# Performance work log

Measured on AMD Instinct MI355X. Metric: run time of the kernel, lower is better.

Reference implementation:

```python
import jax, jax.numpy as jnp
import numpy as np

LN_EPS = 1e-3  # keras LayerNormalization default


def setup_inputs() -> dict:
    key = jax.random.key(0)
    k1, k2, k3 = jax.random.split(key, 3)
    B, T, D, H = 64, 512, 256, 512
    inputs = jax.random.normal(k1, (B, T, D), dtype=jnp.float32)
    h0 = jnp.zeros((B, H), dtype=jnp.float32)
    Wx = jax.random.normal(k2, (D, H), dtype=jnp.float32) / np.sqrt(D)
    Wh = jax.random.normal(k3, (H, H), dtype=jnp.float32) / np.sqrt(H)
    b = jnp.zeros((H,), dtype=jnp.float32)
    gamma = jnp.ones((H,), dtype=jnp.float32)
    beta = jnp.zeros((H,), dtype=jnp.float32)
    return {"inputs": inputs, "h0": h0, "Wx": Wx, "Wh": Wh, "b": b,
            "gamma": gamma, "beta": beta}


def _layer_norm(x, gamma, beta):
    mu = jnp.mean(x, axis=-1, keepdims=True)
    var = jnp.mean(jnp.square(x - mu), axis=-1, keepdims=True)
    return (x - mu) * jax.lax.rsqrt(var + LN_EPS) * gamma + beta


def reference(inputs, h0, Wx, Wh, b, gamma, beta):
    # Precompute input projection for all timesteps: [B, T, H]
    xproj = jnp.einsum('btd,dh->bth', inputs, Wx) + b

    def step(h, xp_t):
        z = xp_t + h @ Wh                      # SimpleRNNCell, activation=None
        h_new = jnp.tanh(_layer_norm(z, gamma, beta))
        return h_new, h_new

    _, outs = jax.lax.scan(step, h0, jnp.swapaxes(xproj, 0, 1))
    return jnp.swapaxes(outs, 0, 1)            # [B, T, H]
```

## Files before the change

kernel.cpp:

```cpp
#include <hip/hip_runtime.h>
#include <cstdint>
#include <cstddef>

#define T_STEPS 512
#define D_DIM 256
#define H_DIM 512
#define B_SZ 64

#define NCG 4
#define CGW (H_DIM / NCG)
#define NTH 512


#define BM 64
#define BN 128
#define BK 32

__global__ __launch_bounds__(256)
void xproj_gemm(const float* __restrict__ A, const float* __restrict__ Bm,
                const float* __restrict__ bias, float* __restrict__ C,
                int M, int N, int K) {
    __shared__ float As[BK][BM];
    __shared__ float Bs[BK][BN];

    const int tid = threadIdx.x;
    const int tx = tid & 15;
    const int ty = tid >> 4;
    const int row0 = blockIdx.y * BM;
    const int col0 = blockIdx.x * BN;

    float acc[4][8];
    #pragma unroll
    for (int i = 0; i < 4; ++i)
        #pragma unroll
        for (int j = 0; j < 8; ++j) acc[i][j] = 0.0f;

    for (int kt = 0; kt < K; kt += BK) {
        #pragma unroll
        for (int i = 0; i < 2; ++i) {
            int q  = tid + i * 256;
            int m  = q >> 3;
            int k4 = (q & 7) << 2;
            float4 v = *(const float4*)&A[(size_t)(row0 + m) * K + kt + k4];
            As[k4 + 0][m] = v.x; As[k4 + 1][m] = v.y;
            As[k4 + 2][m] = v.z; As[k4 + 3][m] = v.w;
        }
        #pragma unroll
        for (int i = 0; i < 4; ++i) {
            int q  = tid + i * 256;
            int kk = q >> 5;
            int n4 = (q & 31) << 2;
            *(float4*)&Bs[kk][n4] = *(const float4*)&Bm[(size_t)(kt + kk) * N + col0 + n4];
        }
        __syncthreads();
        #pragma unroll
        for (int k = 0; k < BK; ++k) {
            float4 a  = *(const float4*)&As[k][ty << 2];
            float4 b0 = *(const float4*)&Bs[k][tx << 2];
            float4 b1 = *(const float4*)&Bs[k][(tx << 2) + 64];
            float av[4] = {a.x, a.y, a.z, a.w};
            float bv[8] = {b0.x, b0.y, b0.z, b0.w, b1.x, b1.y, b1.z, b1.w};
            #pragma unroll
            for (int i = 0; i < 4; ++i)
                #pragma unroll
                for (int j = 0; j < 8; ++j)
                    acc[i][j] = fmaf(av[i], bv[j], acc[i][j]);
        }
        __syncthreads();
    }

    float bv0[4], bv1[4];
    #pragma unroll
    for (int j = 0; j < 4; ++j) {
        bv0[j] = bias[col0 + (tx << 2) + j];
        bv1[j] = bias[col0 + (tx << 2) + 64 + j];
    }
    #pragma unroll
    for (int i = 0; i < 4; ++i) {
        int r = row0 + (ty << 2) + i;
        float4 o0 = make_float4(acc[i][0] + bv0[0], acc[i][1] + bv0[1],
                                acc[i][2] + bv0[2], acc[i][3] + bv0[3]);
        float4 o1 = make_float4(acc[i][4] + bv1[0], acc[i][5] + bv1[1],
                                acc[i][6] + bv1[2], acc[i][7] + bv1[3]);
        *(float4*)&C[(size_t)r * N + col0 + (tx << 2)]      = o0;
        *(float4*)&C[(size_t)r * N + col0 + (tx << 2) + 64] = o1;
    }
}

__device__ __forceinline__ float tanh_fast(float x) {
    float ax = fabsf(x);
    float e  = __expf(2.0f * ax);
    float t  = 1.0f - 2.0f / (e + 1.0f);
    return copysignf(t, x);
}

__global__ __launch_bounds__(NTH)
void rnn_scan3(const float* __restrict__ Wh, const float* __restrict__ h0,
               const float* __restrict__ gamma, const float* __restrict__ beta,
               float* __restrict__ out,
               unsigned long long* __restrict__ zbuf) {
    const int r   = blockIdx.x & (B_SZ - 1);
    const int cg  = blockIdx.x >> 6;
    const int tid = threadIdx.x;
    const int c   = tid & (CGW - 1);
    const int kc  = tid >> 7;

    __shared__ float h_s[H_DIM];
    __shared__ float part_s[NCG][CGW];
    __shared__ float wred_s[16];

    float w[128];
    #pragma unroll
    for (int j = 0; j < 128; ++j)
        w[j] = Wh[(size_t)(kc * 128 + j) * H_DIM + cg * CGW + c];

    h_s[tid] = h0[r * H_DIM + tid];
    const float g_own = gamma[tid];
    const float b_own = beta[tid];
    float* outrow = out + (size_t)r * T_STEPS * H_DIM;
    unsigned long long* zrow0 = zbuf + (size_t)(r * 2) * H_DIM;
    __syncthreads();

    for (int t = 0; t < T_STEPS; ++t) {
        unsigned long long* zrow = zrow0 + (size_t)(t & 1) * H_DIM;
        const unsigned int tag = (unsigned int)(t + 1);

        float xp = 0.0f;
        if (tid < CGW) xp = outrow[t * H_DIM + cg * CGW + tid];

        float acc = 0.0f;
        const float4* h4 = (const float4*)&h_s[kc * 128];
        #pragma unroll
        for (int j4 = 0; j4 < 32; ++j4) {
            float4 hv = h4[j4];
            acc = fmaf(w[4 * j4 + 0], hv.x, acc);
            acc = fmaf(w[4 * j4 + 1], hv.y, acc);
            acc = fmaf(w[4 * j4 + 2], hv.z, acc);
            acc = fmaf(w[4 * j4 + 3], hv.w, acc);
        }
        part_s[kc][c] = acc;
        __syncthreads();

        if (tid < CGW) {
            float z = xp + part_s[0][tid] + part_s[1][tid]
                         + part_s[2][tid] + part_s[3][tid];
            unsigned long long pkt =
                ((unsigned long long)tag << 32) | (unsigned long long)__float_as_uint(z);
            __hip_atomic_store(&zrow[cg * CGW + tid], pkt,
                               __ATOMIC_RELAXED, __HIP_MEMORY_SCOPE_AGENT);
        }

        unsigned long long pkt;
        do {
            pkt = __hip_atomic_load(&zrow[tid], __ATOMIC_RELAXED,
                                    __HIP_MEMORY_SCOPE_AGENT);
        } while ((unsigned int)(pkt >> 32) != tag);
        float z = __uint_as_float((unsigned int)pkt);

        float s = z, q = z * z;
        #pragma unroll
        for (int o = 32; o > 0; o >>= 1) {
            s += __shfl_down(s, o, 64);
            q += __shfl_down(q, o, 64);
        }
        const int wid = tid >> 6;
        if ((tid & 63) == 0) { wred_s[wid] = s; wred_s[8 + wid] = q; }
        __syncthreads();
        float S = 0.0f, Q = 0.0f;
        #pragma unroll
        for (int i = 0; i < 8; ++i) { S += wred_s[i]; Q += wred_s[8 + i]; }
        float mean = S * (1.0f / H_DIM);
        float var  = Q * (1.0f / H_DIM) - mean * mean;
        float rstd = rsqrtf(var + 1e-3f);

        float hn = tanh_fast((z - mean) * rstd * g_own + b_own);
        if (kc == cg) outrow[t * H_DIM + tid] = hn;
        h_s[tid] = hn;
        __syncthreads();
    }
}

extern "C" void kernel_launch(void* const* d_in, const int* in_sizes, int n_in,
                              void* d_out, int out_size, void* d_ws, size_t ws_size,
                              hipStream_t stream) {
    const float* inputs = (const float*)d_in[0];
    const float* h0     = (const float*)d_in[1];
    const float* Wx     = (const float*)d_in[2];
    const float* Wh     = (const float*)d_in[3];
    const float* bias   = (const float*)d_in[4];
    const float* gamma  = (const float*)d_in[5];
    const float* beta   = (const float*)d_in[6];
    float* out = (float*)d_out;

    unsigned long long* zbuf = (unsigned long long*)d_ws;

    const int M = B_SZ * T_STEPS;
    dim3 g1(H_DIM / BN, M / BM);
    xproj_gemm<<<g1, 256, 0, stream>>>(inputs, Wx, bias, out, M, H_DIM, D_DIM);

    rnn_scan3<<<B_SZ * NCG, NTH, 0, stream>>>(Wh, h0, gamma, beta, out, zbuf);
}
```

Measured before the change: 1.246 ms.

## Exchange raw per-slice partials across blocks with fast-poll path and slow fallback

Adds a new scan kernel in which every thread publishes its raw K-slice partial sum to global memory, instead of reducing in shared memory and publishing only the combined column values. Each thread then polls the four partials for its own column and sums them itself, which removes one __syncthreads per step and the part_s shared buffer. Polling first uses plain sc0 loads on a separate buffer, capped at a fixed iteration count, and falls back to agent-scope atomic loads on a mirrored buffer. The kernel also double-buffers h in shared memory, prefetches the next step's xproj, splits the dot product into four accumulators and uses nontemporal stores. In exchange it does four times the global exchange traffic plus duplicate stores, and the fast path depends on non-atomic loads eventually seeing remote writes. The new path runs only when the workspace is at least 4 MB.

```diff
diff --git a/kernel.cpp b/kernel.cpp
--- a/kernel.cpp
+++ b/kernel.cpp
@@ -10,6 +10,7 @@
 #define NCG 4
 #define CGW (H_DIM / NCG)
 #define NTH 512
+#define POLL_CAP 4096
 
 
 #define BM 64
@@ -95,6 +96,135 @@
 }
 
 __global__ __launch_bounds__(NTH)
+void rnn_scan4(const float* __restrict__ Wh, const float* __restrict__ h0,
+               const float* __restrict__ gamma, const float* __restrict__ beta,
+               float* __restrict__ out,
+               unsigned long long* __restrict__ zfast,
+               unsigned long long* __restrict__ zslow) {
+    const int r   = blockIdx.x & (B_SZ - 1);
+    const int cg  = blockIdx.x >> 6;
+    const int tid = threadIdx.x;
+    const int c   = tid & (CGW - 1);
+    const int kc  = tid >> 7;
+
+    __shared__ float h_s[2][H_DIM];
+    __shared__ float wred_s[16];
+
+    float w[128];
+    #pragma unroll
+    for (int j = 0; j < 128; ++j)
+        w[j] = Wh[(size_t)(kc * 128 + j) * H_DIM + cg * CGW + c];
+
+    h_s[0][tid] = h0[r * H_DIM + tid];
+    const float g_own = gamma[tid];
+    const float b_own = beta[tid];
+    float* outrow = out + (size_t)r * T_STEPS * H_DIM;
+
+    unsigned long long* zf0 = zfast + (size_t)r * 2 * (NCG * H_DIM);
+    unsigned long long* zs0 = zslow + (size_t)r * 2 * (NCG * H_DIM);
+    const int pub_off = kc * H_DIM + cg * CGW + c;
+
+    float xp_next = 0.0f;
+    if (tid < CGW)
+        xp_next = __builtin_nontemporal_load(&outrow[cg * CGW + tid]);
+    int fastmode = 1;
+    __syncthreads();
+
+    for (int t = 0; t < T_STEPS; ++t) {
+        unsigned long long* zf = zf0 + (size_t)(t & 1) * (NCG * H_DIM);
+        unsigned long long* zs = zs0 + (size_t)(t & 1) * (NCG * H_DIM);
+        const unsigned int tag = (unsigned int)(t + 1);
+        const float xp = xp_next;
+
+        const float4* h4 = (const float4*)&h_s[t & 1][kc * 128];
+        float a0 = 0.0f, a1 = 0.0f, a2 = 0.0f, a3 = 0.0f;
+        #pragma unroll
+        for (int j4 = 0; j4 < 32; ++j4) {
+            float4 hv = h4[j4];
+            a0 = fmaf(w[4 * j4 + 0], hv.x, a0);
+            a1 = fmaf(w[4 * j4 + 1], hv.y, a1);
+            a2 = fmaf(w[4 * j4 + 2], hv.z, a2);
+            a3 = fmaf(w[4 * j4 + 3], hv.w, a3);
+        }
+        float part = (a0 + a1) + (a2 + a3);
+        if (tid < CGW) part = xp + part;
+
+        const unsigned long long pkt =
+            ((unsigned long long)tag << 32) | (unsigned long long)__float_as_uint(part);
+        asm volatile("global_store_dwordx2 %0, %1, off"
+                     :: "v"(&zf[pub_off]), "v"(pkt) : "memory");
+        __hip_atomic_store(&zs[pub_off], pkt,
+                           __ATOMIC_RELAXED, __HIP_MEMORY_SCOPE_AGENT);
+
+        if (tid < CGW && t + 1 < T_STEPS)
+            xp_next = __builtin_nontemporal_load(
+                &outrow[(size_t)(t + 1) * H_DIM + cg * CGW + tid]);
+
+        unsigned long long p0, p1, p2, p3;
+        bool ok = false;
+        if (fastmode) {
+            const unsigned long long* f0 = &zf[0 * H_DIM + tid];
+            const unsigned long long* f1 = &zf[1 * H_DIM + tid];
+            const unsigned long long* f2 = &zf[2 * H_DIM + tid];
+            const unsigned long long* f3 = &zf[3 * H_DIM + tid];
+            #pragma unroll 1
+            for (int it = 0; it < POLL_CAP; ++it) {
+                asm volatile(
+                    "global_load_dwordx2 %0, %4, off sc0\n\t"
+                    "global_load_dwordx2 %1, %5, off sc0\n\t"
+                    "global_load_dwordx2 %2, %6, off sc0\n\t"
+                    "global_load_dwordx2 %3, %7, off sc0\n\t"
+                    "s_waitcnt vmcnt(0)"
+                    : "=&v"(p0), "=&v"(p1), "=&v"(p2), "=&v"(p3)
+                    : "v"(f0), "v"(f1), "v"(f2), "v"(f3)
+                    : "memory");
+                if ((unsigned)(p0 >> 32) == tag && (unsigned)(p1 >> 32) == tag &&
+                    (unsigned)(p2 >> 32) == tag && (unsigned)(p3 >> 32) == tag) {
+                    ok = true; break;
+                }
+            }
+            if (!ok) fastmode = 0;
+        }
+        if (!ok) {
+            bool g0 = false, g1 = false, g2 = false, g3 = false;
+            do {
+                if (!g0) { unsigned long long v = __hip_atomic_load(&zs[0 * H_DIM + tid], __ATOMIC_RELAXED, __HIP_MEMORY_SCOPE_AGENT); if ((unsigned)(v >> 32) == tag) { p0 = v; g0 = true; } }
+                if (!g1) { unsigned long long v = __hip_atomic_load(&zs[1 * H_DIM + tid], __ATOMIC_RELAXED, __HIP_MEMORY_SCOPE_AGENT); if ((unsigned)(v >> 32) == tag) { p1 = v; g1 = true; } }
+                if (!g2) { unsigned long long v = __hip_atomic_load(&zs[2 * H_DIM + tid], __ATOMIC_RELAXED, __HIP_MEMORY_SCOPE_AGENT); if ((unsigned)(v >> 32) == tag) { p2 = v; g2 = true; } }
+                if (!g3) { unsigned long long v = __hip_atomic_load(&zs[3 * H_DIM + tid], __ATOMIC_RELAXED, __HIP_MEMORY_SCOPE_AGENT); if ((unsigned)(v >> 32) == tag) { p3 = v; g3 = true; } }
+            } while (!(g0 && g1 && g2 && g3));
+        }
+
+        float z = __uint_as_float((unsigned)p0);
+        z += __uint_as_float((unsigned)p1);
+        z += __uint_as_float((unsigned)p2);
+        z += __uint_as_float((unsigned)p3);
+
+        float s = z, q = z * z;
+        #pragma unroll
+        for (int o = 32; o > 0; o >>= 1) {
+            s += __shfl_down(s, o, 64);
+            q += __shfl_down(q, o, 64);
+        }
+        const int wid = tid >> 6;
+        if ((tid & 63) == 0) { wred_s[wid] = s; wred_s[8 + wid] = q; }
+        __syncthreads();
+        float S = 0.0f, Q = 0.0f;
+        #pragma unroll
+        for (int i = 0; i < 8; ++i) { S += wred_s[i]; Q += wred_s[8 + i]; }
+        float mean = S * (1.0f / H_DIM);
+        float var  = Q * (1.0f / H_DIM) - mean * mean;
+        float rstd = rsqrtf(var + 1e-3f);
+
+        float hn = tanh_fast((z - mean) * rstd * g_own + b_own);
+        if (kc == cg)
+            __builtin_nontemporal_store(hn, &outrow[(size_t)t * H_DIM + tid]);
+        h_s[(t & 1) ^ 1][tid] = hn;
+        __syncthreads();
+    }
+}
+
+__global__ __launch_bounds__(NTH)
 void rnn_scan3(const float* __restrict__ Wh, const float* __restrict__ h0,
                const float* __restrict__ gamma, const float* __restrict__ beta,
                float* __restrict__ out,
@@ -192,11 +322,17 @@
     const float* beta   = (const float*)d_in[6];
     float* out = (float*)d_out;
 
-    unsigned long long* zbuf = (unsigned long long*)d_ws;
-
     const int M = B_SZ * T_STEPS;
     dim3 g1(H_DIM / BN, M / BM);
     xproj_gemm<<<g1, 256, 0, stream>>>(inputs, Wx, bias, out, M, H_DIM, D_DIM);
 
-    rnn_scan3<<<B_SZ * NCG, NTH, 0, stream>>>(Wh, h0, gamma, beta, out, zbuf);
-}
+    if (ws_size >= (size_t)(4u << 20)) {
+        unsigned long long* zfast = (unsigned long long*)d_ws;
+        unsigned long long* zslow = zfast + (size_t)B_SZ * 2 * NCG * H_DIM;
+        rnn_scan4<<<B_SZ * NCG, NTH, 0, stream>>>(Wh, h0, gamma, beta, out,
+                                                  zfast, zslow);
+    } else {
+        rnn_scan3<<<B_SZ * NCG, NTH, 0, stream>>>(Wh, h0, gamma, beta, out,
+                                                  (unsigned long long*)d_ws);
+    }
+}
```

Measured after the change: 3.902 ms. 213% more time.

## Process four batch rows per block so register-resident Wh is reused across rows

Applied to the files above, without the earlier changes.

Each block in the recurrent scan now handles four batch rows instead of one. The register-held slice of Wh is reused for four matvecs per step, and the grid drops from 256 to 64 blocks. The final reduction and the publish/poll exchange are spread across all four thread groups, each group publishing one row. It also adds split accumulators, a prefetch of the next step's xproj value, and nontemporal stores. The risk is more serial work per block per step and fewer blocks on the GPU, with polling now on four rows.

```diff
diff --git a/kernel.cpp b/kernel.cpp
--- a/kernel.cpp
+++ b/kernel.cpp
@@ -10,6 +10,8 @@
 #define NCG 4
 #define CGW (H_DIM / NCG)
 #define NTH 512
+#define RPW 4
+#define RGN (B_SZ / RPW)
 
 
 #define BM 64
@@ -94,88 +96,140 @@
     return copysignf(t, x);
 }
 
-__global__ __launch_bounds__(NTH)
-void rnn_scan3(const float* __restrict__ Wh, const float* __restrict__ h0,
+__global__ __launch_bounds__(NTH, 2)
+void rnn_scan5(const float* __restrict__ Wh, const float* __restrict__ h0,
                const float* __restrict__ gamma, const float* __restrict__ beta,
                float* __restrict__ out,
                unsigned long long* __restrict__ zbuf) {
-    const int r   = blockIdx.x & (B_SZ - 1);
-    const int cg  = blockIdx.x >> 6;
+    const int rg  = blockIdx.x & (RGN - 1);
+    const int cg  = blockIdx.x >> 4;
     const int tid = threadIdx.x;
     const int c   = tid & (CGW - 1);
     const int kc  = tid >> 7;
 
-    __shared__ float h_s[H_DIM];
-    __shared__ float part_s[NCG][CGW];
-    __shared__ float wred_s[16];
+    __shared__ float h_s[RPW][H_DIM];
+    __shared__ float part_s[RPW][NCG][CGW];
+    __shared__ float wred_s[RPW][16];
 
     float w[128];
     #pragma unroll
     for (int j = 0; j < 128; ++j)
         w[j] = Wh[(size_t)(kc * 128 + j) * H_DIM + cg * CGW + c];
 
-    h_s[tid] = h0[r * H_DIM + tid];
+    #pragma unroll
+    for (int i = 0; i < RPW; ++i)
+        h_s[i][tid] = h0[(rg + RGN * i) * H_DIM + tid];
+
     const float g_own = gamma[tid];
     const float b_own = beta[tid];
-    float* outrow = out + (size_t)r * T_STEPS * H_DIM;
-    unsigned long long* zrow0 = zbuf + (size_t)(r * 2) * H_DIM;
+
+    const int r_pub = rg + RGN * kc;
+    const float* xp_base = out + (size_t)r_pub * T_STEPS * H_DIM + cg * CGW + c;
+    unsigned long long* zpub = zbuf + (size_t)r_pub * 2 * H_DIM + cg * CGW + c;
+
+    float xp_next = __builtin_nontemporal_load(xp_base);
     __syncthreads();
 
     for (int t = 0; t < T_STEPS; ++t) {
-        unsigned long long* zrow = zrow0 + (size_t)(t & 1) * H_DIM;
+        const size_t par = (size_t)(t & 1) * H_DIM;
         const unsigned int tag = (unsigned int)(t + 1);
-
-        float xp = 0.0f;
-        if (tid < CGW) xp = outrow[t * H_DIM + cg * CGW + tid];
-
-        float acc = 0.0f;
-        const float4* h4 = (const float4*)&h_s[kc * 128];
-        #pragma unroll
-        for (int j4 = 0; j4 < 32; ++j4) {
-            float4 hv = h4[j4];
-            acc = fmaf(w[4 * j4 + 0], hv.x, acc);
-            acc = fmaf(w[4 * j4 + 1], hv.y, acc);
-            acc = fmaf(w[4 * j4 + 2], hv.z, acc);
-            acc = fmaf(w[4 * j4 + 3], hv.w, acc);
-        }
-        part_s[kc][c] = acc;
-        __syncthreads();
-
-        if (tid < CGW) {
-            float z = xp + part_s[0][tid] + part_s[1][tid]
-                         + part_s[2][tid] + part_s[3][tid];
-            unsigned long long pkt =
-                ((unsigned long long)tag << 32) | (unsigned long long)__float_as_uint(z);
-            __hip_atomic_store(&zrow[cg * CGW + tid], pkt,
+        const float xp = xp_next;
+
+        #pragma unroll
+        for (int i = 0; i < RPW; ++i) {
+            const float4* h4 = (const float4*)&h_s[i][kc * 128];
+            float a0 = 0.0f, a1 = 0.0f, a2 = 0.0f, a3 = 0.0f;
+            #pragma unroll
+            for (int j4 = 0; j4 < 32; ++j4) {
+                float4 hv = h4[j4];
+                a0 = fmaf(w[4 * j4 + 0], hv.x, a0);
+                a1 = fmaf(w[4 * j4 + 1], hv.y, a1);
+                a2 = fmaf(w[4 * j4 + 2], hv.z, a2);
+                a3 = fmaf(w[4 * j4 + 3], hv.w, a3);
+            }
+            part_s[i][kc][c] = (a0 + a1) + (a2 + a3);
+        }
+        __syncthreads();
+
+        {
+            float zp = xp + part_s[kc][0][c] + part_s[kc][1][c]
+                          + part_s[kc][2][c] + part_s[kc][3][c];
+            unsigned long long pkt = ((unsigned long long)tag << 32)
+                                   | (unsigned long long)__float_as_uint(zp);
+            __hip_atomic_store(&zpub[par], pkt,
                                __ATOMIC_RELAXED, __HIP_MEMORY_SCOPE_AGENT);
         }
 
-        unsigned long long pkt;
-        do {
-            pkt = __hip_atomic_load(&zrow[tid], __ATOMIC_RELAXED,
-                                    __HIP_MEMORY_SCOPE_AGENT);
-        } while ((unsigned int)(pkt >> 32) != tag);
-        float z = __uint_as_float((unsigned int)pkt);
-
-        float s = z, q = z * z;
+        if (t + 1 < T_STEPS)
+            xp_next = __builtin_nontemporal_load(
+                xp_base + (size_t)(t + 1) * H_DIM);
+
+        float z[RPW];
+        {
+            bool got0 = false, got1 = false, got2 = false, got3 = false;
+            do {
+                if (!got0) {
+                    unsigned long long v = __hip_atomic_load(
+                        &zbuf[(size_t)(rg + 0 * RGN) * 2 * H_DIM + par + tid],
+                        __ATOMIC_RELAXED, __HIP_MEMORY_SCOPE_AGENT);
+                    if ((unsigned)(v >> 32) == tag) { z[0] = __uint_as_float((unsigned)v); got0 = true; }
+                }
+                if (!got1) {
+                    unsigned long long v = __hip_atomic_load(
+                        &zbuf[(size_t)(rg + 1 * RGN) * 2 * H_DIM + par + tid],
+                        __ATOMIC_RELAXED, __HIP_MEMORY_SCOPE_AGENT);
+                    if ((unsigned)(v >> 32) == tag) { z[1] = __uint_as_float((unsigned)v); got1 = true; }
+                }
+                if (!got2) {
+                    unsigned long long v = __hip_atomic_load(
+                        &zbuf[(size_t)(rg + 2 * RGN) * 2 * H_DIM + par + tid],
+                        __ATOMIC_RELAXED, __HIP_MEMORY_SCOPE_AGENT);
+                    if ((unsigned)(v >> 32) == tag) { z[2] = __uint_as_float((unsigned)v); got2 = true; }
+                }
+                if (!got3) {
+                    unsigned long long v = __hip_atomic_load(
+                        &zbuf[(size_t)(rg + 3 * RGN) * 2 * H_DIM + par + tid],
+                        __ATOMIC_RELAXED, __HIP_MEMORY_SCOPE_AGENT);
+                    if ((unsigned)(v >> 32) == tag) { z[3] = __uint_as_float((unsigned)v); got3 = true; }
+                }
+            } while (!(got0 && got1 && got2 && got3));
+        }
+
+        float s[RPW], q[RPW];
+        #pragma unroll
+        for (int i = 0; i < RPW; ++i) { s[i] = z[i]; q[i] = z[i] * z[i]; }
         #pragma unroll
         for (int o = 32; o > 0; o >>= 1) {
-            s += __shfl_down(s, o, 64);
-            q += __shfl_down(q, o, 64);
+            #pragma unroll
+            for (int i = 0; i < RPW; ++i) {
+                s[i] += __shfl_down(s[i], o, 64);
+                q[i] += __shfl_down(q[i], o, 64);
+            }
         }
         const int wid = tid >> 6;
-        if ((tid & 63) == 0) { wred_s[wid] = s; wred_s[8 + wid] = q; }
-        __syncthreads();
-        float S = 0.0f, Q = 0.0f;
-        #pragma unroll
-        for (int i = 0; i < 8; ++i) { S += wred_s[i]; Q += wred_s[8 + i]; }
-        float mean = S * (1.0f / H_DIM);
-        float var  = Q * (1.0f / H_DIM) - mean * mean;
-        float rstd = rsqrtf(var + 1e-3f);
-
-        float hn = tanh_fast((z - mean) * rstd * g_own + b_own);
-        if (kc == cg) outrow[t * H_DIM + tid] = hn;
-        h_s[tid] = hn;
+        if ((tid & 63) == 0) {
+            #pragma unroll
+            for (int i = 0; i < RPW; ++i) {
+                wred_s[i][wid]     = s[i];
+                wred_s[i][8 + wid] = q[i];
+            }
+        }
+        __syncthreads();
+
+        #pragma unroll
+        for (int i = 0; i < RPW; ++i) {
+            float S = 0.0f, Q = 0.0f;
+            #pragma unroll
+            for (int k = 0; k < 8; ++k) { S += wred_s[i][k]; Q += wred_s[i][8 + k]; }
+            float mean = S * (1.0f / H_DIM);
+            float var  = Q * (1.0f / H_DIM) - mean * mean;
+            float rstd = rsqrtf(var + 1e-3f);
+            float hn = tanh_fast((z[i] - mean) * rstd * g_own + b_own);
+            if (kc == cg)
+                __builtin_nontemporal_store(hn,
+                    &out[((size_t)(rg + RGN * i) * T_STEPS + t) * H_DIM + tid]);
+            h_s[i][tid] = hn;
+        }
         __syncthreads();
     }
 }
@@ -198,5 +252,5 @@
     dim3 g1(H_DIM / BN, M / BM);
     xproj_gemm<<<g1, 256, 0, stream>>>(inputs, Wx, bias, out, M, H_DIM, D_DIM);
 
-    rnn_scan3<<<B_SZ * NCG, NTH, 0, stream>>>(Wh, h0, gamma, beta, out, zbuf);
-}
+    rnn_scan5<<<RGN * NCG, NTH, 0, stream>>>(Wh, h0, gamma, beta, out, zbuf);
+}
```

After: 3.171 ms. +154.6%, slower.

## Split recurrent matvec over eight column groups with prefetched input projection

Applied to the files above, without the earlier changes.

Each batch row's hidden columns are now split across 8 cooperating blocks instead of 4, halving the register-resident Wh slice per thread to 64 values and the dot length per thread. The dot product uses four independent accumulators to break the FMA dependency chain. The next timestep's input projection is prefetched with nontemporal loads while blocks wait on the cross-block exchange, and outputs are written with nontemporal stores. The cost is twice as many blocks spinning on the global exchange buffer each step, and more partial sums to reduce per step.

```diff
diff --git a/kernel.cpp b/kernel.cpp
--- a/kernel.cpp
+++ b/kernel.cpp
@@ -7,7 +7,7 @@
 #define H_DIM 512
 #define B_SZ 64
 
-#define NCG 4
+#define NCG 8
 #define CGW (H_DIM / NCG)
 #define NTH 512
 
@@ -94,61 +94,68 @@
     return copysignf(t, x);
 }
 
-__global__ __launch_bounds__(NTH)
-void rnn_scan3(const float* __restrict__ Wh, const float* __restrict__ h0,
+__global__ __launch_bounds__(NTH, 4)
+void rnn_scan6(const float* __restrict__ Wh, const float* __restrict__ h0,
                const float* __restrict__ gamma, const float* __restrict__ beta,
                float* __restrict__ out,
                unsigned long long* __restrict__ zbuf) {
-    const int r   = blockIdx.x & (B_SZ - 1);
-    const int cg  = blockIdx.x >> 6;
+    const int cg  = blockIdx.x & (NCG - 1);
+    const int r   = blockIdx.x >> 3;
     const int tid = threadIdx.x;
     const int c   = tid & (CGW - 1);
-    const int kc  = tid >> 7;
+    const int kc  = tid >> 6;
 
     __shared__ float h_s[H_DIM];
     __shared__ float part_s[NCG][CGW];
     __shared__ float wred_s[16];
 
-    float w[128];
-    #pragma unroll
-    for (int j = 0; j < 128; ++j)
-        w[j] = Wh[(size_t)(kc * 128 + j) * H_DIM + cg * CGW + c];
+    float w[64];
+    #pragma unroll
+    for (int j = 0; j < 64; ++j)
+        w[j] = Wh[(size_t)(kc * CGW + j) * H_DIM + cg * CGW + c];
 
     h_s[tid] = h0[r * H_DIM + tid];
     const float g_own = gamma[tid];
     const float b_own = beta[tid];
     float* outrow = out + (size_t)r * T_STEPS * H_DIM;
     unsigned long long* zrow0 = zbuf + (size_t)(r * 2) * H_DIM;
+
+    float xp_next = 0.0f;
+    if (tid < CGW)
+        xp_next = __builtin_nontemporal_load(&outrow[cg * CGW + tid]);
     __syncthreads();
 
     for (int t = 0; t < T_STEPS; ++t) {
         unsigned long long* zrow = zrow0 + (size_t)(t & 1) * H_DIM;
         const unsigned int tag = (unsigned int)(t + 1);
-
-        float xp = 0.0f;
-        if (tid < CGW) xp = outrow[t * H_DIM + cg * CGW + tid];
-
-        float acc = 0.0f;
-        const float4* h4 = (const float4*)&h_s[kc * 128];
-        #pragma unroll
-        for (int j4 = 0; j4 < 32; ++j4) {
+        const float xp = xp_next;
+
+        const float4* h4 = (const float4*)&h_s[kc * CGW];
+        float a0 = 0.0f, a1 = 0.0f, a2 = 0.0f, a3 = 0.0f;
+        #pragma unroll
+        for (int j4 = 0; j4 < 16; ++j4) {
             float4 hv = h4[j4];
-            acc = fmaf(w[4 * j4 + 0], hv.x, acc);
-            acc = fmaf(w[4 * j4 + 1], hv.y, acc);
-            acc = fmaf(w[4 * j4 + 2], hv.z, acc);
-            acc = fmaf(w[4 * j4 + 3], hv.w, acc);
-        }
-        part_s[kc][c] = acc;
+            a0 = fmaf(w[4 * j4 + 0], hv.x, a0);
+            a1 = fmaf(w[4 * j4 + 1], hv.y, a1);
+            a2 = fmaf(w[4 * j4 + 2], hv.z, a2);
+            a3 = fmaf(w[4 * j4 + 3], hv.w, a3);
+        }
+        part_s[kc][c] = (a0 + a1) + (a2 + a3);
         __syncthreads();
 
         if (tid < CGW) {
-            float z = xp + part_s[0][tid] + part_s[1][tid]
-                         + part_s[2][tid] + part_s[3][tid];
-            unsigned long long pkt =
-                ((unsigned long long)tag << 32) | (unsigned long long)__float_as_uint(z);
+            float z = xp;
+            #pragma unroll
+            for (int k = 0; k < NCG; ++k) z += part_s[k][tid];
+            unsigned long long pkt = ((unsigned long long)tag << 32)
+                                   | (unsigned long long)__float_as_uint(z);
             __hip_atomic_store(&zrow[cg * CGW + tid], pkt,
                                __ATOMIC_RELAXED, __HIP_MEMORY_SCOPE_AGENT);
         }
+
+        if (tid < CGW && t + 1 < T_STEPS)
+            xp_next = __builtin_nontemporal_load(
+                &outrow[(size_t)(t + 1) * H_DIM + cg * CGW + tid]);
 
         unsigned long long pkt;
         do {
@@ -163,8 +170,7 @@
             s += __shfl_down(s, o, 64);
             q += __shfl_down(q, o, 64);
         }
-        const int wid = tid >> 6;
-        if ((tid & 63) == 0) { wred_s[wid] = s; wred_s[8 + wid] = q; }
+        if ((tid & 63) == 0) { wred_s[kc] = s; wred_s[8 + kc] = q; }
         __syncthreads();
         float S = 0.0f, Q = 0.0f;
         #pragma unroll
@@ -174,7 +180,8 @@
         float rstd = rsqrtf(var + 1e-3f);
 
         float hn = tanh_fast((z - mean) * rstd * g_own + b_own);
-        if (kc == cg) outrow[t * H_DIM + tid] = hn;
+        if (kc == cg)
+            __builtin_nontemporal_store(hn, &outrow[(size_t)t * H_DIM + tid]);
         h_s[tid] = hn;
         __syncthreads();
     }
@@ -198,5 +205,5 @@
     dim3 g1(H_DIM / BN, M / BM);
     xproj_gemm<<<g1, 256, 0, stream>>>(inputs, Wx, bias, out, M, H_DIM, D_DIM);
 
-    rnn_scan3<<<B_SZ * NCG, NTH, 0, stream>>>(Wh, h0, gamma, beta, out, zbuf);
-}
+    rnn_scan6<<<B_SZ * NCG, NTH, 0, stream>>>(Wh, h0, gamma, beta, out, zbuf);
+}
```

New measurement: 1.265 ms. Within noise of the previous version (+1.6%).
